# Kernel tuning notes

Measured on AMD Instinct MI355X. Metric: run time of the kernel, lower is better.

Reference implementation:

```python
import jax, jax.numpy as jnp
import numpy as np

N, T, L = 4, 2048, 2048
DQIN, DFEAT, DQK, DV = 32, 34, 64, 64  # modality feat=34 -> V input = 34-2 = 32, K input = last col


def _sorted_timeline(k, shape):
    return jnp.sort(jax.random.uniform(k, shape, jnp.float32) * 100.0, axis=-1)


def setup_inputs() -> dict:
    key = jax.random.key(0)
    ks = jax.random.split(key, 32)
    inp = {}
    inp["ref_data"] = jax.random.normal(ks[0], (N, 1, T, DQIN), jnp.float32)
    inp["ref_t"] = _sorted_timeline(ks[1], (N, 1, T))
    inp["m1_data"] = jax.random.normal(ks[2], (N, 1, L, DFEAT), jnp.float32)
    inp["m1_t"] = _sorted_timeline(ks[3], (N, 1, L))
    inp["m2_data"] = jax.random.normal(ks[4], (N, 1, L, DFEAT), jnp.float32)
    inp["m2_t"] = _sorted_timeline(ks[5], (N, 1, L))
    inp["m3_data"] = jax.random.normal(ks[6], (N, 1, L, DFEAT), jnp.float32)
    inp["m3_t"] = _sorted_timeline(ks[7], (N, 1, L))
    # shared W_Q (bias=False): d_q_in -> d_qk
    inp["Wq"] = jax.random.normal(ks[8], (DQIN, DQK), jnp.float32) / np.sqrt(DQIN)
    # per-modality params: W_K: 1 -> d_qk (with bias), W_V: (DFEAT-2) -> d_v (with bias), log-temperature
    for i, m in enumerate(["1", "2", "3"]):
        b = 9 + 4 * i
        inp["Wk" + m] = jax.random.normal(ks[b], (1, DQK), jnp.float32)
        inp["bk" + m] = jax.random.normal(ks[b + 1], (DQK,), jnp.float32) * 0.02
        inp["Wv" + m] = jax.random.normal(ks[b + 2], (DFEAT - 2, DV), jnp.float32) / np.sqrt(DFEAT - 2)
        inp["bv" + m] = jax.random.normal(ks[b + 3], (DV,), jnp.float32) * 0.02
        inp["log_tau" + m] = jnp.zeros((), jnp.float32)  # log(init_tau=1)
    return inp


def _unimodal(Q, ref_t, data, t, Wk, bk, Wv, bv, log_tau):
    # K path: last feature column through linear, then feature_map_k = [1, -x]
    Kr = data[..., -1:] @ Wk + bk                                   # (N,1,L,DQK)
    K = jnp.concatenate([jnp.ones(Kr.shape[:-1] + (1,), Kr.dtype), -Kr], axis=-1)  # (N,1,L,DQK+1)
    V = data[..., :-2] @ Wv + bv                                    # (N,1,L,DV)
    tau = jnp.exp(log_tau)
    # gaussian weight: -(Q.K)^2 / tau
    S = -jnp.square(jnp.einsum('nhtc,nhlc->nhtl', Q, K)) / tau       # (N,1,T,L)
    mask = (ref_t[..., :, None] >= t[..., None, :]).astype(S.dtype)  # (N,1,T,L)
    A = jax.nn.softmax(S * mask, axis=-1) * mask
    return jnp.einsum('nhtl,nhlc->nhtc', A, V)                       # (N,1,T,DV)


def reference(ref_data, ref_t, m1_data, m1_t, m2_data, m2_t, m3_data, m3_t,
              Wq, Wk1, bk1, Wv1, bv1, log_tau1, Wk2, bk2, Wv2, bv2, log_tau2,
              Wk3, bk3, Wv3, bv3, log_tau3):
    # compute_Q (qk_type='time'): Q = add_one(W_Q(ref_data)) -> append ones column
    Qr = jnp.einsum('nhtd,dk->nhtk', ref_data, Wq)
    Q = jnp.concatenate([Qr, jnp.ones(Qr.shape[:-1] + (1,), Qr.dtype)], axis=-1)  # (N,1,T,DQK+1)
    y1 = _unimodal(Q, ref_t, m1_data, m1_t, Wk1, bk1, Wv1, bv1, log_tau1)
    y2 = _unimodal(Q, ref_t, m2_data, m2_t, Wk2, bk2, Wv2, bv2, log_tau2)
    y3 = _unimodal(Q, ref_t, m3_data, m3_t, Wk3, bk3, Wv3, bv3, log_tau3)
    # original returns dict {m1: y1, m2: y2, m3: y3}; stacked here (3,N,1,T,DV)
    return jnp.stack([y1, y2, y3], axis=0)
```

## Files before the change

kernel.cpp:

```cpp
#include <hip/hip_runtime.h>

namespace {

typedef unsigned int uint;
typedef unsigned short ushort_t;
typedef __attribute__((ext_vector_type(8))) short bf16x8;
typedef __attribute__((ext_vector_type(4))) float f32x4;

constexpr int N = 4, T = 2048, L = 2048;
constexpr int DQIN = 32, DQK = 64;

constexpr int VI_SZ = 3 * N * 64 * L;
constexpr int X_SZ = 3 * N * L;
constexpr int A_SZ = 3 * N * T;

union PK8 { int i[4]; bf16x8 s; };

__global__ __launch_bounds__(256) void mm_prep(
    const float* __restrict__ ref_data, const float* __restrict__ ref_t,
    const float* __restrict__ d1, const float* __restrict__ t1,
    const float* __restrict__ d2, const float* __restrict__ t2,
    const float* __restrict__ d3, const float* __restrict__ t3,
    const float* __restrict__ Wq,
    const float* __restrict__ Wk1, const float* __restrict__ bk1,
    const float* __restrict__ Wv1, const float* __restrict__ bv1, const float* __restrict__ lt1,
    const float* __restrict__ Wk2, const float* __restrict__ bk2,
    const float* __restrict__ Wv2, const float* __restrict__ bv2, const float* __restrict__ lt2,
    const float* __restrict__ Wk3, const float* __restrict__ bk3,
    const float* __restrict__ Wv3, const float* __restrict__ bv3, const float* __restrict__ lt3,
    float* __restrict__ Aq, float* __restrict__ Gq, int* __restrict__ Cq,
    ushort_t* __restrict__ VI, float* __restrict__ X) {
  const int b = blockIdx.x;
  const int tid = threadIdx.x;

  if (b < 96) {
    const int m = b >> 5;
    const int idx = (b & 31) * 256 + tid;
    __shared__ float sWq[DQIN * DQK];
    __shared__ float sWk[DQK];
    __shared__ float sbk[DQK];
    const float* Wk = (m == 0) ? Wk1 : (m == 1 ? Wk2 : Wk3);
    const float* bk = (m == 0) ? bk1 : (m == 1 ? bk2 : bk3);
    const float* lt = (m == 0) ? lt1 : (m == 1 ? lt2 : lt3);
    for (int i = tid; i < DQIN * DQK; i += 256) sWq[i] = Wq[i];
    if (tid < DQK) { sWk[tid] = Wk[tid]; sbk[tid] = bk[tid]; }
    __syncthreads();
    float x[DQIN];
    const float* rp = ref_data + idx * DQIN;
#pragma unroll
    for (int i = 0; i < DQIN; i++) x[i] = rp[i];
    float qr[DQK];
#pragma unroll
    for (int j = 0; j < DQK; j += 4) {
      float4 acc4 = make_float4(0.f, 0.f, 0.f, 0.f);
#pragma unroll
      for (int i = 0; i < DQIN; i++) {
        const float4 w = *(const float4*)&sWq[i * DQK + j];
        acc4.x = fmaf(x[i], w.x, acc4.x);
        acc4.y = fmaf(x[i], w.y, acc4.y);
        acc4.z = fmaf(x[i], w.z, acc4.z);
        acc4.w = fmaf(x[i], w.w, acc4.w);
      }
      qr[j] = acc4.x; qr[j + 1] = acc4.y; qr[j + 2] = acc4.z; qr[j + 3] = acc4.w;
    }
    const float rs = __expf(-0.5f * lt[0]);
    float g = 0.f, h = 0.f;
#pragma unroll
    for (int j = 1; j < DQK; j++) {
      g = fmaf(qr[j], sWk[j - 1], g);
      h = fmaf(qr[j], sbk[j - 1], h);
    }
    g += sWk[DQK - 1];
    h += sbk[DQK - 1];
    Aq[m * (N * T) + idx] = (qr[0] - h) * rs;
    Gq[m * (N * T) + idx] = g * rs;
  } else if (b < 192) {
    const int sidx = (b - 96) * 256 + tid;
    const int m = sidx >> 13;
    const int nt = sidx & 8191;
    const int n = nt >> 11;
    const float rt = ref_t[nt];
    const float* tml = ((m == 0) ? t1 : (m == 1 ? t2 : t3)) + n * L;
    int lo = 0, hi = L;
    while (lo < hi) {
      const int mid = (lo + hi) >> 1;
      if (tml[mid] <= rt) lo = mid + 1; else hi = mid;
    }
    Cq[m * 8192 + nt] = lo;
  } else {
    const int vb = b - 192;
    const int mn = vb >> 5;
    const int m = mn >> 2, n = mn & 3;
    const int lseg0 = (vb & 31) * 64;
    const float* dm = (m == 0) ? d1 : (m == 1 ? d2 : d3);
    const float* Wv = (m == 0) ? Wv1 : (m == 1 ? Wv2 : Wv3);
    const float* bv = (m == 0) ? bv1 : (m == 1 ? bv2 : bv3);
    const int cdim = tid & 63;
    const int qq = tid >> 6;
    const int l0 = lseg0 + qq * 16;

    float Wc[32];
#pragma unroll
    for (int i = 0; i < 32; i++) Wc[i] = Wv[i * 64 + cdim];
    const float bvc = bv[cdim];

    uint hi16[16], lo16[16];
#pragma unroll 4
    for (int k = 0; k < 16; k++) {
      const float* dp = dm + (size_t)(n * L + l0 + k) * 34;
      float acc = bvc;
#pragma unroll
      for (int i = 0; i < 32; i++) acc = fmaf(dp[i], Wc[i], acc);
      uint u = __float_as_uint(acc);
      uint h = (u + 0x7fffu + ((u >> 16) & 1u)) & 0xffff0000u;
      float res = acc - __uint_as_float(h);
      uint ul = __float_as_uint(res);
      uint hl = (ul + 0x7fffu + ((ul >> 16) & 1u)) >> 16;
      hi16[k] = h >> 16;
      lo16[k] = hl;
    }
    int pkh[8], pkl[8];
#pragma unroll
    for (int p = 0; p < 8; p++) {
      pkh[p] = (int)(hi16[2 * p] | (hi16[2 * p + 1] << 16));
      pkl[p] = (int)(lo16[2 * p] | (lo16[2 * p + 1] << 16));
    }
    ushort_t* dst = VI + (size_t)(mn * 64 + cdim) * (2 * L) + (l0 >> 3) * 16;
    *(int4*)dst = make_int4(pkh[0], pkh[1], pkh[2], pkh[3]);
    *(int4*)(dst + 8) = make_int4(pkl[0], pkl[1], pkl[2], pkl[3]);
    *(int4*)(dst + 16) = make_int4(pkh[4], pkh[5], pkh[6], pkh[7]);
    *(int4*)(dst + 24) = make_int4(pkl[4], pkl[5], pkl[6], pkl[7]);

    if (tid < 64) {
      const int l = lseg0 + tid;
      X[mn * L + l] = dm[(size_t)(n * L + l) * 34 + 33];
    }
  }
}

__device__ inline void stage_chunk(ushort_t* dstbuf, const ushort_t* VIb, int ch,
                                   int w, int lane) {
#pragma unroll
  for (int i = 0; i < 8; i++) {
    const int n = (w * 8 + i) * 64 + lane;
    const int lr = n >> 5;
    const int slot = n & 31;
    const int u = (slot - lr) & 31;
    const ushort_t* src = VIb + (size_t)lr * 4096 + ch * 256 + u * 8;
    __builtin_amdgcn_global_load_lds(
        (const __attribute__((address_space(1))) void*)src,
        (__attribute__((address_space(3))) void*)(dstbuf + (w * 8 + i) * 512),
        16, 0, 0);
  }
}

__global__ __launch_bounds__(128, 2) void mm_attn_main(
    const ushort_t* __restrict__ VI, const float* __restrict__ X,
    const float* __restrict__ Aq, const float* __restrict__ Gq, const int* __restrict__ Cq,
    float* __restrict__ out) {
  __shared__ ushort_t sbuf[2][8192];
  __shared__ float sx[2048];

  const int b = blockIdx.x;
  const int mn = b % 12;
  const int rr0 = b / 12;
  const int dh = rr0 & 1;
  const int j = rr0 >> 1;
  const int pj = 63 - j;

  const int tid = threadIdx.x;
  const int lane = tid & 63;
  const int w = tid >> 6;
  const int q = lane >> 4;
  const int m16 = lane & 15;

  const int rg = pj * 2 + w;
  const int tbase = mn * T + rg * 16;

  const int c = Cq[tbase + m16];
  const int cmax = __shfl(c, 15, 64);
  const int cmin = __shfl(c, 0, 64);
  const int nch = (cmax + 127) >> 7;

  const int cB = Cq[mn * T + (pj * 2 + 1) * 16 + 15];
  const int nchB = (cB + 127) >> 7;

  const float a = Aq[tbase + m16];
  const float g = Gq[tbase + m16];

  f32x4 acc[2];
  acc[0] = (f32x4){0.f, 0.f, 0.f, 0.f};
  acc[1] = (f32x4){0.f, 0.f, 0.f, 0.f};
  float z = 0.f;

  const ushort_t* VIb = VI + (size_t)(mn * 64 + dh * 32) * 4096;
  const float* xg = X + mn * L;

  int oh[2][4], ol[2][4];
#pragma unroll
  for (int ct = 0; ct < 2; ct++) {
#pragma unroll
    for (int kk = 0; kk < 4; kk++) {
      const int lr = ct * 16 + m16;
      const int uh = (kk * 4 + q) * 2;
      oh[ct][kk] = lr * 256 + (((uh + 0) + lr) & 31) * 8;
      ol[ct][kk] = lr * 256 + (((uh + 1) + lr) & 31) * 8;
    }
  }

#pragma unroll
  for (int i = 0; i < 4; i++) {
    const float* src = xg + (w * 4 + i) * 256 + lane * 4;
    __builtin_amdgcn_global_load_lds(
        (const __attribute__((address_space(1))) void*)src,
        (__attribute__((address_space(3))) void*)(sx + (w * 4 + i) * 256),
        16, 0, 0);
  }
  stage_chunk(sbuf[0], VIb, 0, w, lane);
  __syncthreads();

  for (int ch = 0; ch < nchB; ch++) {
    const int nb = ch & 1;
    if (ch + 1 < nchB) stage_chunk(sbuf[nb ^ 1], VIb, ch + 1, w, lane);

    if (ch < nch) {
      const int base = ch << 7;
      const ushort_t* buf = sbuf[nb];
      const bool inter = (base + 128 <= cmin);
#pragma unroll
      for (int kk = 0; kk < 4; kk++) {
        const int k0 = base + kk * 32 + q * 8;
        const float4 xa = *(const float4*)&sx[k0];
        const float4 xb = *(const float4*)&sx[k0 + 4];
        const float xs[8] = {xa.x, xa.y, xa.z, xa.w, xb.x, xb.y, xb.z, xb.w};
        float wv[8];
        if (inter) {
#pragma unroll
          for (int jj = 0; jj < 8; jj++) {
            const float d = fmaf(-g, xs[jj], a);
            wv[jj] = __expf(-d * d);
            z += wv[jj];
          }
        } else {
#pragma unroll
          for (int jj = 0; jj < 8; jj++) {
            const float d = fmaf(-g, xs[jj], a);
            const float e = __expf(-d * d);
            wv[jj] = (k0 + jj < c) ? e : 0.f;
            z += wv[jj];
          }
        }
        PK8 ph, pl;
#pragma unroll
        for (int p2 = 0; p2 < 4; p2++) {
          const uint u0 = __float_as_uint(wv[2 * p2]);
          const uint u1 = __float_as_uint(wv[2 * p2 + 1]);
          const uint h0 = u0 & 0xffff0000u, h1 = u1 & 0xffff0000u;
          const float l0f = wv[2 * p2] - __uint_as_float(h0);
          const float l1f = wv[2 * p2 + 1] - __uint_as_float(h1);
          ph.i[p2] = (int)((h0 >> 16) | h1);
          pl.i[p2] = (int)((__float_as_uint(l0f) >> 16) | (__float_as_uint(l1f) & 0xffff0000u));
        }
        const bf16x8 ahi = ph.s, alo = pl.s;
#pragma unroll
        for (int ct = 0; ct < 2; ct++) {
          const bf16x8 bh = *(const bf16x8*)(buf + oh[ct][kk]);
          const bf16x8 bl = *(const bf16x8*)(buf + ol[ct][kk]);
          acc[ct] = __builtin_amdgcn_mfma_f32_16x16x32_bf16(ahi, bh, acc[ct], 0, 0, 0);
          acc[ct] = __builtin_amdgcn_mfma_f32_16x16x32_bf16(ahi, bl, acc[ct], 0, 0, 0);
          acc[ct] = __builtin_amdgcn_mfma_f32_16x16x32_bf16(alo, bh, acc[ct], 0, 0, 0);
        }
      }
    }
    __syncthreads();
  }

  z += __shfl_xor(z, 16, 64);
  z += __shfl_xor(z, 32, 64);

#pragma unroll
  for (int rr = 0; rr < 4; rr++) {
    const int row = q * 4 + rr;
    const float zr = __shfl(z, row, 64);
    const int cr = __shfl(c, row, 64);
    const float inv = 1.0f / (zr + (float)(L - cr));
#pragma unroll
    for (int ct = 0; ct < 2; ct++) {
      out[(size_t)(tbase + row) * 64 + dh * 32 + ct * 16 + m16] = acc[ct][rr] * inv;
    }
  }
}

}

extern "C" void kernel_launch(void* const* d_in, const int* in_sizes, int n_in,
                              void* d_out, int out_size, void* d_ws, size_t ws_size,
                              hipStream_t stream) {
  const float* ref_data = (const float*)d_in[0];
  const float* ref_t = (const float*)d_in[1];
  const float* m1_data = (const float*)d_in[2];
  const float* m1_t = (const float*)d_in[3];
  const float* m2_data = (const float*)d_in[4];
  const float* m2_t = (const float*)d_in[5];
  const float* m3_data = (const float*)d_in[6];
  const float* m3_t = (const float*)d_in[7];
  const float* Wq = (const float*)d_in[8];
  const float* Wk1 = (const float*)d_in[9];
  const float* bk1 = (const float*)d_in[10];
  const float* Wv1 = (const float*)d_in[11];
  const float* bv1 = (const float*)d_in[12];
  const float* lt1 = (const float*)d_in[13];
  const float* Wk2 = (const float*)d_in[14];
  const float* bk2 = (const float*)d_in[15];
  const float* Wv2 = (const float*)d_in[16];
  const float* bv2 = (const float*)d_in[17];
  const float* lt2 = (const float*)d_in[18];
  const float* Wk3 = (const float*)d_in[19];
  const float* bk3 = (const float*)d_in[20];
  const float* Wv3 = (const float*)d_in[21];
  const float* bv3 = (const float*)d_in[22];
  const float* lt3 = (const float*)d_in[23];

  float* ws = (float*)d_ws;
  ushort_t* VI = (ushort_t*)ws;
  float* Xw = ws + VI_SZ;
  float* Aq = Xw + X_SZ;
  float* Gq = Aq + A_SZ;
  int* Cq = (int*)(Gq + A_SZ);

  mm_prep<<<dim3(576), dim3(256), 0, stream>>>(
      ref_data, ref_t, m1_data, m1_t, m2_data, m2_t, m3_data, m3_t, Wq,
      Wk1, bk1, Wv1, bv1, lt1, Wk2, bk2, Wv2, bv2, lt2, Wk3, bk3, Wv3, bv3, lt3,
      Aq, Gq, Cq, VI, Xw);
  mm_attn_main<<<dim3(12 * 64 * 2), dim3(128), 0, stream>>>(
      VI, Xw, Aq, Gq, Cq, (float*)d_out);
}
```

Measured before the change: 150.1 us.

## Compute both V halves per block, reusing softmax weights across halves

Each block now covers all 64 output columns instead of splitting them into two halves across blocks. The exp-weight computation and bf16 hi/lo split are done once per chunk and reused for both halves. The two LDS buffers now hold the two halves of the same chunk rather than double-buffering successive chunks. This removes the duplicated exp work and halves the grid to 768 blocks, but it adds an extra barrier per chunk, reduces overlap of loads with compute, and raises register pressure.

```diff
diff --git a/kernel.cpp b/kernel.cpp
--- a/kernel.cpp
+++ b/kernel.cpp
@@ -163,9 +163,7 @@
 
   const int b = blockIdx.x;
   const int mn = b % 12;
-  const int rr0 = b / 12;
-  const int dh = rr0 & 1;
-  const int j = rr0 >> 1;
+  const int j = b / 12;
   const int pj = 63 - j;
 
   const int tid = threadIdx.x;
@@ -188,12 +186,13 @@
   const float a = Aq[tbase + m16];
   const float g = Gq[tbase + m16];
 
-  f32x4 acc[2];
-  acc[0] = (f32x4){0.f, 0.f, 0.f, 0.f};
-  acc[1] = (f32x4){0.f, 0.f, 0.f, 0.f};
+  f32x4 acc[4];
+#pragma unroll
+  for (int i = 0; i < 4; i++) acc[i] = (f32x4){0.f, 0.f, 0.f, 0.f};
   float z = 0.f;
 
-  const ushort_t* VIb = VI + (size_t)(mn * 64 + dh * 32) * 4096;
+  const ushort_t* VIh0 = VI + (size_t)(mn * 64) * 4096;
+  const ushort_t* VIh1 = VI + (size_t)(mn * 64 + 32) * 4096;
   const float* xg = X + mn * L;
 
   int oh[2][4], ol[2][4];
@@ -216,16 +215,16 @@
         (__attribute__((address_space(3))) void*)(sx + (w * 4 + i) * 256),
         16, 0, 0);
   }
-  stage_chunk(sbuf[0], VIb, 0, w, lane);
+  stage_chunk(sbuf[0], VIh0, 0, w, lane);
   __syncthreads();
 
   for (int ch = 0; ch < nchB; ch++) {
-    const int nb = ch & 1;
-    if (ch + 1 < nchB) stage_chunk(sbuf[nb ^ 1], VIb, ch + 1, w, lane);
-
+    stage_chunk(sbuf[1], VIh1, ch, w, lane);
+
+    bf16x8 sh[4], sl[4];
     if (ch < nch) {
       const int base = ch << 7;
-      const ushort_t* buf = sbuf[nb];
+      const ushort_t* buf = sbuf[0];
       const bool inter = (base + 128 <= cmin);
 #pragma unroll
       for (int kk = 0; kk < 4; kk++) {
@@ -261,14 +260,33 @@
           ph.i[p2] = (int)((h0 >> 16) | h1);
           pl.i[p2] = (int)((__float_as_uint(l0f) >> 16) | (__float_as_uint(l1f) & 0xffff0000u));
         }
-        const bf16x8 ahi = ph.s, alo = pl.s;
+        sh[kk] = ph.s;
+        sl[kk] = pl.s;
 #pragma unroll
         for (int ct = 0; ct < 2; ct++) {
           const bf16x8 bh = *(const bf16x8*)(buf + oh[ct][kk]);
           const bf16x8 bl = *(const bf16x8*)(buf + ol[ct][kk]);
-          acc[ct] = __builtin_amdgcn_mfma_f32_16x16x32_bf16(ahi, bh, acc[ct], 0, 0, 0);
-          acc[ct] = __builtin_amdgcn_mfma_f32_16x16x32_bf16(ahi, bl, acc[ct], 0, 0, 0);
-          acc[ct] = __builtin_amdgcn_mfma_f32_16x16x32_bf16(alo, bh, acc[ct], 0, 0, 0);
+          acc[ct] = __builtin_amdgcn_mfma_f32_16x16x32_bf16(sh[kk], bh, acc[ct], 0, 0, 0);
+          acc[ct] = __builtin_amdgcn_mfma_f32_16x16x32_bf16(sh[kk], bl, acc[ct], 0, 0, 0);
+          acc[ct] = __builtin_amdgcn_mfma_f32_16x16x32_bf16(sl[kk], bh, acc[ct], 0, 0, 0);
+        }
+      }
+    }
+    __syncthreads();
+
+    if (ch + 1 < nchB) stage_chunk(sbuf[0], VIh0, ch + 1, w, lane);
+
+    if (ch < nch) {
+      const ushort_t* buf = sbuf[1];
+#pragma unroll
+      for (int kk = 0; kk < 4; kk++) {
+#pragma unroll
+        for (int ct = 0; ct < 2; ct++) {
+          const bf16x8 bh = *(const bf16x8*)(buf + oh[ct][kk]);
+          const bf16x8 bl = *(const bf16x8*)(buf + ol[ct][kk]);
+          acc[2 + ct] = __builtin_amdgcn_mfma_f32_16x16x32_bf16(sh[kk], bh, acc[2 + ct], 0, 0, 0);
+          acc[2 + ct] = __builtin_amdgcn_mfma_f32_16x16x32_bf16(sh[kk], bl, acc[2 + ct], 0, 0, 0);
+          acc[2 + ct] = __builtin_amdgcn_mfma_f32_16x16x32_bf16(sl[kk], bh, acc[2 + ct], 0, 0, 0);
         }
       }
     }
@@ -285,8 +303,12 @@
     const int cr = __shfl(c, row, 64);
     const float inv = 1.0f / (zr + (float)(L - cr));
 #pragma unroll
-    for (int ct = 0; ct < 2; ct++) {
-      out[(size_t)(tbase + row) * 64 + dh * 32 + ct * 16 + m16] = acc[ct][rr] * inv;
+    for (int hh = 0; hh < 2; hh++) {
+#pragma unroll
+      for (int ct = 0; ct < 2; ct++) {
+        out[(size_t)(tbase + row) * 64 + hh * 32 + ct * 16 + m16] =
+            acc[hh * 2 + ct][rr] * inv;
+      }
     }
   }
 }
@@ -332,6 +354,6 @@
       ref_data, ref_t, m1_data, m1_t, m2_data, m2_t, m3_data, m3_t, Wq,
       Wk1, bk1, Wv1, bv1, lt1, Wk2, bk2, Wv2, bv2, lt2, Wk3, bk3, Wv3, bv3, lt3,
       Aq, Gq, Cq, VI, Xw);
-  mm_attn_main<<<dim3(12 * 64 * 2), dim3(128), 0, stream>>>(
+  mm_attn_main<<<dim3(12 * 64), dim3(128), 0, stream>>>(
       VI, Xw, Aq, Gq, Cq, (float*)d_out);
 }
```

Result: slower. 156.8 us (+4.5%).

## Drop LDS staging and read V directly from global with full-width blocks

Applied to the files above, without the earlier changes.

The attention kernel no longer stages V chunks and x values into shared memory with async global-to-LDS loads and barriers. Each wave now loads its MFMA B operands straight from global memory (relying on L1/L2), processes all 64 output columns per block instead of splitting them across two blocks, and iterates in 64-wide chunks. This removes LDS traffic, barriers and the duplicate exponent computation across the two column halves, but loses the double-buffered prefetch and exposes global-load latency, with fewer blocks in the grid.

```diff
diff --git a/kernel.cpp b/kernel.cpp
--- a/kernel.cpp
+++ b/kernel.cpp
@@ -138,34 +138,13 @@
   }
 }
 
-__device__ inline void stage_chunk(ushort_t* dstbuf, const ushort_t* VIb, int ch,
-                                   int w, int lane) {
-#pragma unroll
-  for (int i = 0; i < 8; i++) {
-    const int n = (w * 8 + i) * 64 + lane;
-    const int lr = n >> 5;
-    const int slot = n & 31;
-    const int u = (slot - lr) & 31;
-    const ushort_t* src = VIb + (size_t)lr * 4096 + ch * 256 + u * 8;
-    __builtin_amdgcn_global_load_lds(
-        (const __attribute__((address_space(1))) void*)src,
-        (__attribute__((address_space(3))) void*)(dstbuf + (w * 8 + i) * 512),
-        16, 0, 0);
-  }
-}
-
-__global__ __launch_bounds__(128, 2) void mm_attn_main(
+__global__ __launch_bounds__(128) void mm_attn_main(
     const ushort_t* __restrict__ VI, const float* __restrict__ X,
     const float* __restrict__ Aq, const float* __restrict__ Gq, const int* __restrict__ Cq,
     float* __restrict__ out) {
-  __shared__ ushort_t sbuf[2][8192];
-  __shared__ float sx[2048];
-
   const int b = blockIdx.x;
   const int mn = b % 12;
-  const int rr0 = b / 12;
-  const int dh = rr0 & 1;
-  const int j = rr0 >> 1;
+  const int j = b / 12;
   const int pj = 63 - j;
 
   const int tid = threadIdx.x;
@@ -180,99 +159,81 @@
   const int c = Cq[tbase + m16];
   const int cmax = __shfl(c, 15, 64);
   const int cmin = __shfl(c, 0, 64);
-  const int nch = (cmax + 127) >> 7;
-
-  const int cB = Cq[mn * T + (pj * 2 + 1) * 16 + 15];
-  const int nchB = (cB + 127) >> 7;
+  const int nch = (cmax + 63) >> 6;
 
   const float a = Aq[tbase + m16];
   const float g = Gq[tbase + m16];
 
-  f32x4 acc[2];
-  acc[0] = (f32x4){0.f, 0.f, 0.f, 0.f};
-  acc[1] = (f32x4){0.f, 0.f, 0.f, 0.f};
+  f32x4 acc[4];
+#pragma unroll
+  for (int i = 0; i < 4; i++) acc[i] = (f32x4){0.f, 0.f, 0.f, 0.f};
   float z = 0.f;
 
-  const ushort_t* VIb = VI + (size_t)(mn * 64 + dh * 32) * 4096;
   const float* xg = X + mn * L;
 
-  int oh[2][4], ol[2][4];
-#pragma unroll
-  for (int ct = 0; ct < 2; ct++) {
-#pragma unroll
-    for (int kk = 0; kk < 4; kk++) {
-      const int lr = ct * 16 + m16;
-      const int uh = (kk * 4 + q) * 2;
-      oh[ct][kk] = lr * 256 + (((uh + 0) + lr) & 31) * 8;
-      ol[ct][kk] = lr * 256 + (((uh + 1) + lr) & 31) * 8;
-    }
-  }
-
-#pragma unroll
-  for (int i = 0; i < 4; i++) {
-    const float* src = xg + (w * 4 + i) * 256 + lane * 4;
-    __builtin_amdgcn_global_load_lds(
-        (const __attribute__((address_space(1))) void*)src,
-        (__attribute__((address_space(3))) void*)(sx + (w * 4 + i) * 256),
-        16, 0, 0);
-  }
-  stage_chunk(sbuf[0], VIb, 0, w, lane);
-  __syncthreads();
-
-  for (int ch = 0; ch < nchB; ch++) {
-    const int nb = ch & 1;
-    if (ch + 1 < nchB) stage_chunk(sbuf[nb ^ 1], VIb, ch + 1, w, lane);
-
-    if (ch < nch) {
-      const int base = ch << 7;
-      const ushort_t* buf = sbuf[nb];
-      const bool inter = (base + 128 <= cmin);
-#pragma unroll
-      for (int kk = 0; kk < 4; kk++) {
-        const int k0 = base + kk * 32 + q * 8;
-        const float4 xa = *(const float4*)&sx[k0];
-        const float4 xb = *(const float4*)&sx[k0 + 4];
-        const float xs[8] = {xa.x, xa.y, xa.z, xa.w, xb.x, xb.y, xb.z, xb.w};
-        float wv[8];
-        if (inter) {
-#pragma unroll
-          for (int jj = 0; jj < 8; jj++) {
-            const float d = fmaf(-g, xs[jj], a);
-            wv[jj] = __expf(-d * d);
-            z += wv[jj];
-          }
-        } else {
-#pragma unroll
-          for (int jj = 0; jj < 8; jj++) {
-            const float d = fmaf(-g, xs[jj], a);
-            const float e = __expf(-d * d);
-            wv[jj] = (k0 + jj < c) ? e : 0.f;
-            z += wv[jj];
-          }
+  const ushort_t* Vq[4];
+#pragma unroll
+  for (int hh = 0; hh < 2; hh++)
+#pragma unroll
+    for (int ct = 0; ct < 2; ct++)
+      Vq[hh * 2 + ct] =
+          VI + (size_t)(mn * 64 + hh * 32 + ct * 16 + m16) * 4096 + q * 16;
+
+  for (int ch = 0; ch < nch; ch++) {
+    const int base = ch << 6;
+    const bool inter = (base + 64 <= cmin);
+#pragma unroll
+    for (int kk = 0; kk < 2; kk++) {
+      const int k0 = base + kk * 32 + q * 8;
+      const float4 xa = *(const float4*)&xg[k0];
+      const float4 xb = *(const float4*)&xg[k0 + 4];
+      const float xs[8] = {xa.x, xa.y, xa.z, xa.w, xb.x, xb.y, xb.z, xb.w};
+      float wv[8];
+      if (inter) {
+#pragma unroll
+        for (int jj = 0; jj < 8; jj++) {
+          const float d = fmaf(-g, xs[jj], a);
+          wv[jj] = __expf(-d * d);
+          z += wv[jj];
         }
-        PK8 ph, pl;
-#pragma unroll
-        for (int p2 = 0; p2 < 4; p2++) {
-          const uint u0 = __float_as_uint(wv[2 * p2]);
-          const uint u1 = __float_as_uint(wv[2 * p2 + 1]);
-          const uint h0 = u0 & 0xffff0000u, h1 = u1 & 0xffff0000u;
-          const float l0f = wv[2 * p2] - __uint_as_float(h0);
-          const float l1f = wv[2 * p2 + 1] - __uint_as_float(h1);
-          ph.i[p2] = (int)((h0 >> 16) | h1);
-          pl.i[p2] = (int)((__float_as_uint(l0f) >> 16) | (__float_as_uint(l1f) & 0xffff0000u));
+      } else {
+#pragma unroll
+        for (int jj = 0; jj < 8; jj++) {
+          const float d = fmaf(-g, xs[jj], a);
+          const float e = __expf(-d * d);
+          wv[jj] = (k0 + jj < c) ? e : 0.f;
+          z += wv[jj];
         }
-        const bf16x8 ahi = ph.s, alo = pl.s;
+      }
+      PK8 ph, pl;
+#pragma unroll
+      for (int p2 = 0; p2 < 4; p2++) {
+        const uint u0 = __float_as_uint(wv[2 * p2]);
+        const uint u1 = __float_as_uint(wv[2 * p2 + 1]);
+        const uint h0 = u0 & 0xffff0000u, h1 = u1 & 0xffff0000u;
+        const float l0f = wv[2 * p2] - __uint_as_float(h0);
+        const float l1f = wv[2 * p2 + 1] - __uint_as_float(h1);
+        ph.i[p2] = (int)((h0 >> 16) | h1);
+        pl.i[p2] = (int)((__float_as_uint(l0f) >> 16) | (__float_as_uint(l1f) & 0xffff0000u));
+      }
+      const bf16x8 ahi = ph.s, alo = pl.s;
+      const int goff = (ch * 8 + kk * 4) * 16;
+#pragma unroll
+      for (int hh = 0; hh < 2; hh++) {
 #pragma unroll
         for (int ct = 0; ct < 2; ct++) {
-          const bf16x8 bh = *(const bf16x8*)(buf + oh[ct][kk]);
-          const bf16x8 bl = *(const bf16x8*)(buf + ol[ct][kk]);
-          acc[ct] = __builtin_amdgcn_mfma_f32_16x16x32_bf16(ahi, bh, acc[ct], 0, 0, 0);
-          acc[ct] = __builtin_amdgcn_mfma_f32_16x16x32_bf16(ahi, bl, acc[ct], 0, 0, 0);
-          acc[ct] = __builtin_amdgcn_mfma_f32_16x16x32_bf16(alo, bh, acc[ct], 0, 0, 0);
+          const ushort_t* p = Vq[hh * 2 + ct] + goff;
+          const bf16x8 bh = *(const bf16x8*)p;
+          const bf16x8 bl = *(const bf16x8*)(p + 8);
+          acc[hh * 2 + ct] =
+              __builtin_amdgcn_mfma_f32_16x16x32_bf16(ahi, bh, acc[hh * 2 + ct], 0, 0, 0);
+          acc[hh * 2 + ct] =
+              __builtin_amdgcn_mfma_f32_16x16x32_bf16(ahi, bl, acc[hh * 2 + ct], 0, 0, 0);
+          acc[hh * 2 + ct] =
+              __builtin_amdgcn_mfma_f32_16x16x32_bf16(alo, bh, acc[hh * 2 + ct], 0, 0, 0);
         }
       }
     }
-    __syncthreads();
   }
 
   z += __shfl_xor(z, 16, 64);
@@ -285,8 +246,12 @@
     const int cr = __shfl(c, row, 64);
     const float inv = 1.0f / (zr + (float)(L - cr));
 #pragma unroll
-    for (int ct = 0; ct < 2; ct++) {
-      out[(size_t)(tbase + row) * 64 + dh * 32 + ct * 16 + m16] = acc[ct][rr] * inv;
+    for (int hh = 0; hh < 2; hh++) {
+#pragma unroll
+      for (int ct = 0; ct < 2; ct++) {
+        out[(size_t)(tbase + row) * 64 + hh * 32 + ct * 16 + m16] =
+            acc[hh * 2 + ct][rr] * inv;
+      }
     }
   }
 }
@@ -332,6 +297,6 @@
       ref_data, ref_t, m1_data, m1_t, m2_data, m2_t, m3_data, m3_t, Wq,
       Wk1, bk1, Wv1, bv1, lt1, Wk2, bk2, Wv2, bv2, lt2, Wk3, bk3, Wv3, bv3, lt3,
       Aq, Gq, Cq, VI, Xw);
-  mm_attn_main<<<dim3(12 * 64 * 2), dim3(128), 0, stream>>>(
+  mm_attn_main<<<dim3(12 * 64), dim3(128), 0, stream>>>(
       VI, Xw, Aq, Gq, Cq, (float*)d_out);
 }
```

New measurement: 209.8 us. 39.8% more time.
